# Kernel tuning notes

Hardware: AMD Instinct MI355X
Metric: run time of the kernel (lower is better)

## Reference

```python
import jax, jax.numpy as jnp
import numpy as np

N_QUBITS = 10
N_LAYERS = 3
TWO_PI = np.float32(2.0 * np.pi)


def _apply_1q(state, m, wire, n):
    """Apply 2x2 unitary m to qubit `wire` (wire 0 = MSB) of state [B, 2^n]."""
    B = state.shape[0]
    st = state.reshape(B, 2 ** wire, 2, 2 ** (n - wire - 1))
    st = jnp.einsum('pq,bxqy->bxpy', m, st)
    return st.reshape(B, -1)


def _rot(angles):
    # PennyLane Rot(phi, theta, omega) = RZ(omega) @ RY(theta) @ RZ(phi)
    phi, theta, omega = angles[0], angles[1], angles[2]
    c = jnp.cos(theta / 2)
    s = jnp.sin(theta / 2)
    ep = jnp.exp(-0.5j * (phi + omega))
    em = jnp.exp(-0.5j * (phi - omega))
    return jnp.stack([jnp.stack([ep * c, -jnp.conj(em) * s]),
                      jnp.stack([em * s, jnp.conj(ep) * c])])


def _rot_layer(state, w, n):
    # StronglyEntanglingLayers single-layer Rot block: one Rot per wire. w: [n, 3]
    for j in range(n):
        state = _apply_1q(state, _rot(w[j]), j, n)
    return state


def _circuit(x, weights1, weights2):
    n = N_QUBITS
    B = x.shape[0]
    dim = 2 ** n
    idx = jnp.arange(dim)
    # bits[k, j]: value of qubit j in basis state k (wire 0 = MSB)
    bits = ((idx[:, None] >> (n - 1 - jnp.arange(n)[None, :])) & 1).astype(jnp.float32)
    signs = 1.0 - 2.0 * bits                       # eigenvalues of Z per wire, [dim, n]
    # ring of CZ entanglers (range-1, layer index 0): CZ(i, (i+1) % n) for all i
    pair = bits * jnp.roll(bits, -1, axis=1)
    cz = (1.0 - 2.0 * (jnp.sum(pair, axis=1) % 2.0))  # diagonal, [dim]

    state = jnp.zeros((B, dim), jnp.complex64).at[:, 0].set(1.0)

    for l in range(N_LAYERS):
        state = _rot_layer(state, weights1[l, 0], n)   # StronglyEntanglingLayers Rot block
        state = state * cz[None, :]                    # CZ ring (diagonal)
        # data re-uploading: RZ(x_j) on wire j, all wires fused into one diagonal phase
        state = state * jnp.exp(-0.5j * (x @ signs.T))
    state = _rot_layer(state, weights2[0], n)          # final entangling layer
    state = state * cz[None, :]

    probs = state.real ** 2 + state.imag ** 2          # [B, dim]
    return probs @ signs                               # <Z_j> per wire, [B, n]


def setup_inputs() -> dict:
    key = jax.random.key(0)
    k1, k2, k3 = jax.random.split(key, 3)
    x = jax.random.uniform(k1, (2048, N_QUBITS), jnp.float32) * TWO_PI
    weights1 = jax.random.uniform(k2, (N_LAYERS, 1, N_QUBITS, 3), jnp.float32) * TWO_PI
    weights2 = jax.random.uniform(k3, (1, N_QUBITS, 3), jnp.float32) * TWO_PI
    return {"x": x, "weights1": weights1, "weights2": weights2}


def reference(x, weights1, weights2):
    return _circuit(x, weights1, weights2)
```

## Files before the change

kernel.cpp:

```cpp
#include <hip/hip_runtime.h>
#include <math.h>

#define NQ 10

typedef float v2f __attribute__((ext_vector_type(2)));

static __device__ __forceinline__ v2f mk2(float a, float b) { v2f r; r.x = a; r.y = b; return r; }
static __device__ __forceinline__ v2f sp2(float a)          { v2f r; r.x = a; r.y = a; return r; }
static __device__ __forceinline__ v2f pkfma(v2f a, v2f b, v2f c) { return __builtin_elementwise_fma(a, b, c); }

template<int MSK>
static __device__ __forceinline__ float lxor(float v) {
    if constexpr (MSK == 1) {
        const int s = __float_as_int(v);
        return __int_as_float(__builtin_amdgcn_update_dpp(s, s, 0xB1, 0xF, 0xF, false));
    } else if constexpr (MSK == 2) {
        const int s = __float_as_int(v);
        return __int_as_float(__builtin_amdgcn_update_dpp(s, s, 0x4E, 0xF, 0xF, false));
    } else if constexpr (MSK == 4) {
        const int s = __float_as_int(v);
        int t = __builtin_amdgcn_update_dpp(s, s, 0x104, 0xF, 0x5, false);
        t     = __builtin_amdgcn_update_dpp(t, s, 0x114, 0xF, 0xA, false);
        return __int_as_float(t);
    } else if constexpr (MSK == 8) {
        const int s = __float_as_int(v);
        return __int_as_float(__builtin_amdgcn_update_dpp(s, s, 0x128, 0xF, 0xF, false));
    } else if constexpr (MSK == 16) {
        return __int_as_float(__builtin_amdgcn_ds_swizzle(__float_as_int(v), 0x401F));
    } else {
        return __shfl_xor(v, 32, 64);
    }
}
template<int MSK>
static __device__ __forceinline__ v2f lxor2(v2f v) { return mk2(lxor<MSK>(v.x), lxor<MSK>(v.y)); }

#define PLS32(a, b) asm("v_permlane32_swap_b32 %0, %1" : "+v"(a), "+v"(b))
#define PLS16(a, b) asm("v_permlane16_swap_b32 %0, %1" : "+v"(a), "+v"(b))

__global__ void qlayer_kernel(
    const float* __restrict__ x,
    const float* __restrict__ w1,
    const float* __restrict__ w2,
    float* __restrict__ out)
{
    __shared__ float ry[4 * 20];
    __shared__ float au[3 * 10];

    const int t    = threadIdx.x;
    const int lane = t & 63;
    const int w    = t >> 6;
    const int b    = (blockIdx.x << 2) + w;

    if (t < 40) {
        const int L = t / 10, j = t - L * 10;
        const float th = (L < 3) ? w1[L * 30 + j * 3 + 1] : w2[j * 3 + 1];
        float c, s;
        __sincosf(0.5f * th, &s, &c);
        ry[L * 20 + j * 2 + 0] = c;
        ry[L * 20 + j * 2 + 1] = s;
    } else if (t >= 64 && t < 94) {
        const int i = t - 64, L = i / 10, j = i - L * 10;
        au[i] = w1[L * 30 + j * 3 + 2] + ((L < 2) ? w1[(L + 1) * 30 + j * 3] : w2[j * 3]);
    }

    float xv[NQ];
#pragma unroll
    for (int j = 0; j < NQ; ++j) xv[j] = x[b * NQ + j];

    int msk[4];
#pragma unroll
    for (int p = 0; p < 4; ++p) msk[p] = ((lane >> p) & 1) ? 0 : 0x80000000;

    float czm[16];
#pragma unroll
    for (int m = 0; m < 16; ++m) {
        const int k  = (m << 6) | lane;
        const int kr = ((k << 1) | (k >> 9)) & 1023;
        czm[m] = (__popc(k & kr) & 1) ? -1.f : 1.f;
    }

    __syncthreads();

    v2f dr[8], di[8];
#define BUILD_D(IDX)                                                                   \
    {                                                                                  \
        float A[NQ];                                                                   \
        _Pragma("unroll")                                                              \
        for (int j = 0; j < NQ; ++j) A[j] = au[(IDX) * 10 + j] + xv[j];                \
        float SA = 0.f;                                                                \
        _Pragma("unroll")                                                              \
        for (int j = 0; j < NQ; ++j) SA += A[j];                                       \
        float Tl = 0.f;                                                                \
        _Pragma("unroll")                                                              \
        for (int p = 0; p < 6; ++p) Tl += ((lane >> p) & 1) ? A[9 - p] : 0.f;          \
        const float base = -0.5f * SA + Tl;                                            \
        float fr[4], fi[4];                                                            \
        _Pragma("unroll")                                                              \
        for (int q = 0; q < 4; ++q) __sincosf(A[3 - q], &fi[q], &fr[q]);               \
        float dmr[16], dmi[16];                                                        \
        __sincosf(base, &dmi[0], &dmr[0]);                                             \
        _Pragma("unroll")                                                              \
        for (int m = 1; m < 16; ++m) {                                                 \
            const int q  = (m & 1) ? 0 : (m & 2) ? 1 : (m & 4) ? 2 : 3;                \
            const int pm = m & (m - 1);                                                \
            dmr[m] = dmr[pm] * fr[q] - dmi[pm] * fi[q];                                \
            dmi[m] = dmr[pm] * fi[q] + dmi[pm] * fr[q];                                \
        }                                                                              \
        _Pragma("unroll")                                                              \
        for (int p = 0; p < 8; ++p) {                                                  \
            dr[p] = mk2(dmr[2*p] * czm[2*p], dmr[2*p+1] * czm[2*p+1]);                 \
            di[p] = mk2(dmi[2*p] * czm[2*p], dmi[2*p+1] * czm[2*p+1]);                 \
        }                                                                              \
    }

    float Plo = 1.f;
#pragma unroll
    for (int p = 0; p < 6; ++p) {
        const float cc = ry[(9 - p) * 2], ss = ry[(9 - p) * 2 + 1];
        Plo *= ((lane >> p) & 1) ? ss : cc;
    }
    float Pm[16];
    {
        const float c0 = ry[0], s0 = ry[1], c1 = ry[2], s1 = ry[3];
        const float c2 = ry[4], s2 = ry[5], c3 = ry[6], s3 = ry[7];
        float P2[2] = {c3, s3};
        float P4[4], P8[8];
#pragma unroll
        for (int m = 0; m < 4; ++m)  P4[m] = ((m >> 1) ? s2 : c2) * P2[m & 1];
#pragma unroll
        for (int m = 0; m < 8; ++m)  P8[m] = ((m >> 2) ? s1 : c1) * P4[m & 3];
#pragma unroll
        for (int m = 0; m < 16; ++m) Pm[m] = ((m >> 3) ? s0 : c0) * P8[m & 7];
    }

    BUILD_D(0)
    v2f sr[8], si[8];
#pragma unroll
    for (int p = 0; p < 8; ++p) {
        const v2f pv = sp2(Plo) * mk2(Pm[2 * p], Pm[2 * p + 1]);
        sr[p] = pv * dr[p];
        si[p] = pv * di[p];
    }

#define RY_LANE(J, MSK)                                                         \
    {                                                                           \
        const float c = rl[(J) * 2], s = rl[(J) * 2 + 1];                       \
        const float ssg = __int_as_float(__float_as_int(s) ^ msk[9 - (J)]);     \
        const v2f C = sp2(c), S = sp2(ssg);                                     \
        _Pragma("unroll")                                                       \
        for (int p = 0; p < 8; ++p) {                                           \
            const v2f qr = lxor2<MSK>(sr[p]);                                   \
            const v2f qi = lxor2<MSK>(si[p]);                                   \
            sr[p] = pkfma(C, sr[p], S * qr);                                    \
            si[p] = pkfma(C, si[p], S * qi);                                    \
        }                                                                       \
    }

#define RY_PLPAIR(J, PLS)                                                       \
    {                                                                           \
        const float c = rl[(J) * 2], s = rl[(J) * 2 + 1];                       \
        const v2f C = sp2(c), S = sp2(s), nS = sp2(-s);                         \
        _Pragma("unroll")                                                       \
        for (int p = 0; p < 8; ++p) {                                           \
            float ux = sr[p].x, uy = sr[p].y;                                   \
            float vx = si[p].x, vy = si[p].y;                                   \
            PLS(ux, vx); PLS(uy, vy);                                           \
            const v2f u = mk2(ux, uy), v = mk2(vx, vy);                         \
            const v2f t1 = pkfma(C, u, nS * v);                                 \
            const v2f t2 = pkfma(C, v,  S * u);                                 \
            float ax = t1.x, ay = t1.y, bx = t2.x, by = t2.y;                   \
            PLS(ax, bx); PLS(ay, by);                                           \
            sr[p] = mk2(ax, ay); si[p] = mk2(bx, by);                           \
        }                                                                       \
    }

#pragma unroll 1
    for (int L = 1; L <= 3; ++L) {
        const float* rl = ry + L * 20;

        RY_PLPAIR(4, PLS32)
        RY_PLPAIR(5, PLS16)
        RY_LANE(6, 8)
        RY_LANE(7, 4)
        RY_LANE(8, 2)
        RY_LANE(9, 1)

#pragma unroll
        for (int j = 0; j < 3; ++j) {
            const int pb = 4 >> j;
            const float c = rl[j * 2], s = rl[j * 2 + 1];
            const v2f C = sp2(c), S = sp2(s), nS = sp2(-s);
#pragma unroll
            for (int p0 = 0; p0 < 8; ++p0) {
                if (p0 & pb) continue;
                const int p1 = p0 | pb;
                const v2f a0r = sr[p0], a1r = sr[p1];
                const v2f a0i = si[p0], a1i = si[p1];
                sr[p0] = pkfma(C, a0r, nS * a1r);
                sr[p1] = pkfma(C, a1r,  S * a0r);
                si[p0] = pkfma(C, a0i, nS * a1i);
                si[p1] = pkfma(C, a1i,  S * a0i);
            }
        }

        {
            const float c = rl[6], s = rl[7];
            const v2f C = sp2(c), Sw = mk2(-s, s);
#pragma unroll
            for (int p = 0; p < 8; ++p) {
                const v2f swr = mk2(sr[p].y, sr[p].x);
                const v2f swi = mk2(si[p].y, si[p].x);
                sr[p] = pkfma(C, sr[p], Sw * swr);
                si[p] = pkfma(C, si[p], Sw * swi);
            }
        }

        if (L < 3) {
            BUILD_D(L)
#pragma unroll
            for (int p = 0; p < 8; ++p) {
                const v2f tr = pkfma(sr[p], dr[p], -(si[p] * di[p]));
                si[p] = pkfma(sr[p], di[p], si[p] * dr[p]);
                sr[p] = tr;
            }
        }
    }
#undef RY_LANE
#undef RY_PLPAIR
#undef BUILD_D

    float pe[8], po[8];
#pragma unroll
    for (int p = 0; p < 8; ++p) {
        const v2f pk = pkfma(sr[p], sr[p], si[p] * si[p]);
        pe[p] = pk.x + pk.y;
        po[p] = pk.x - pk.y;
    }
    float tot = 0.f, t0 = 0.f, t1 = 0.f, t2 = 0.f, t3 = 0.f;
#pragma unroll
    for (int p = 0; p < 8; ++p) {
        tot += pe[p];
        t0  += (p & 4) ? -pe[p] : pe[p];
        t1  += (p & 2) ? -pe[p] : pe[p];
        t2  += (p & 1) ? -pe[p] : pe[p];
        t3  += po[p];
    }
    v2f u01 = mk2(t0, t1), u23 = mk2(t2, t3);
    u01 += lxor2<1>(u01);  u23 += lxor2<1>(u23);
    u01 += lxor2<2>(u01);  u23 += lxor2<2>(u23);
    u01 += lxor2<4>(u01);  u23 += lxor2<4>(u23);
    u01 += lxor2<8>(u01);  u23 += lxor2<8>(u23);
    u01 += lxor2<16>(u01); u23 += lxor2<16>(u23);
    u01 += lxor2<32>(u01); u23 += lxor2<32>(u23);

    float Sa = tot, T, D0, D1, D2, D3, D4, D5;
    T = lxor<1>(Sa);  D0 = Sa - T; Sa += T;
    T = lxor<2>(Sa);  D1 = Sa - T; Sa += T;
    T = lxor<4>(Sa);  D2 = Sa - T; Sa += T;
    T = lxor<8>(Sa);  D3 = Sa - T; Sa += T;
    T = lxor<16>(Sa); D4 = Sa - T; Sa += T;
    T = lxor<32>(Sa); D5 = Sa - T;
    D0 += lxor<2>(D0); D0 += lxor<4>(D0); D0 += lxor<8>(D0); D0 += lxor<16>(D0); D0 += lxor<32>(D0);
    D1 += lxor<4>(D1); D1 += lxor<8>(D1); D1 += lxor<16>(D1); D1 += lxor<32>(D1);
    D2 += lxor<8>(D2); D2 += lxor<16>(D2); D2 += lxor<32>(D2);
    D3 += lxor<16>(D3); D3 += lxor<32>(D3);
    D4 += lxor<32>(D4);

    if (lane == 0) {
        float* o = out + b * NQ;
        o[0] = u01.x; o[1] = u01.y; o[2] = u23.x; o[3] = u23.y;
        o[4] = D5;    o[5] = D4;    o[6] = D3;    o[7] = D2;    o[8] = D1;    o[9] = D0;
    }
}

extern "C" void kernel_launch(void* const* d_in, const int* in_sizes, int n_in,
                              void* d_out, int out_size, void* d_ws, size_t ws_size,
                              hipStream_t stream) {
    const float* x  = (const float*)d_in[0];
    const float* w1 = (const float*)d_in[1];
    const float* w2 = (const float*)d_in[2];
    float* out = (float*)d_out;
    const int B = in_sizes[0] / NQ;
    qlayer_kernel<<<B / 4, 256, 0, stream>>>(x, w1, w2, out);
}
```

Measured before the change: 17.77 us.

## Fully unroll layer loop, add launch bounds, scalarize some lane rotations

```diff
diff --git a/kernel.cpp b/kernel.cpp
--- a/kernel.cpp
+++ b/kernel.cpp
@@ -37,7 +37,7 @@
 #define PLS32(a, b) asm("v_permlane32_swap_b32 %0, %1" : "+v"(a), "+v"(b))
 #define PLS16(a, b) asm("v_permlane16_swap_b32 %0, %1" : "+v"(a), "+v"(b))
 
-__global__ void qlayer_kernel(
+__global__ __launch_bounds__(256, 2) void qlayer_kernel(
     const float* __restrict__ x,
     const float* __restrict__ w1,
     const float* __restrict__ w2,
@@ -49,7 +49,7 @@
     const int t    = threadIdx.x;
     const int lane = t & 63;
     const int w    = t >> 6;
-    const int b    = (blockIdx.x << 2) + w;
+    const int b    = __builtin_amdgcn_readfirstlane((blockIdx.x << 2) + w);
 
     if (t < 40) {
         const int L = t / 10, j = t - L * 10;
@@ -142,7 +142,24 @@
         si[p] = pv * di[p];
     }
 
-#define RY_LANE(J, MSK)                                                         \
+#define RY_LANE_S(J, MSK)                                                       \
+    {                                                                           \
+        const float c = rl[(J) * 2], s = rl[(J) * 2 + 1];                       \
+        const float ssg = __int_as_float(__float_as_int(s) ^ msk[9 - (J)]);     \
+        _Pragma("unroll")                                                       \
+        for (int p = 0; p < 8; ++p) {                                           \
+            const float qx = lxor<MSK>(sr[p].x);                                \
+            const float qy = lxor<MSK>(sr[p].y);                                \
+            const float rx = lxor<MSK>(si[p].x);                                \
+            const float ryv = lxor<MSK>(si[p].y);                               \
+            sr[p].x = fmaf(qx,  ssg, c * sr[p].x);                              \
+            sr[p].y = fmaf(qy,  ssg, c * sr[p].y);                              \
+            si[p].x = fmaf(rx,  ssg, c * si[p].x);                              \
+            si[p].y = fmaf(ryv, ssg, c * si[p].y);                              \
+        }                                                                       \
+    }
+
+#define RY_LANE_V(J, MSK)                                                       \
     {                                                                           \
         const float c = rl[(J) * 2], s = rl[(J) * 2 + 1];                       \
         const float ssg = __int_as_float(__float_as_int(s) ^ msk[9 - (J)]);     \
@@ -174,16 +191,16 @@
         }                                                                       \
     }
 
-#pragma unroll 1
+#pragma unroll
     for (int L = 1; L <= 3; ++L) {
         const float* rl = ry + L * 20;
 
         RY_PLPAIR(4, PLS32)
         RY_PLPAIR(5, PLS16)
-        RY_LANE(6, 8)
-        RY_LANE(7, 4)
-        RY_LANE(8, 2)
-        RY_LANE(9, 1)
+        RY_LANE_S(6, 8)
+        RY_LANE_V(7, 4)
+        RY_LANE_S(8, 2)
+        RY_LANE_S(9, 1)
 
 #pragma unroll
         for (int j = 0; j < 3; ++j) {
@@ -225,7 +242,8 @@
             }
         }
     }
-#undef RY_LANE
+#undef RY_LANE_S
+#undef RY_LANE_V
 #undef RY_PLPAIR
 #undef BUILD_D
 
```

Measured after the change: 17.81 us. No clear change (+0.2%).
